# Performance work log

Hardware: AMD Instinct MI355X
Metric: run time of the kernel (lower is better)

The kernel has to match this reference:

```python
import jax, jax.numpy as jnp
import numpy as np

B, DIM, T = 8, 512, 4096
INTER = 1536
K = 7
DIL = 1
EPS = 1e-6
LS_INIT = 1e-6


def _ste(x, q):
    # straight-through estimator: forward uses q, gradient flows through x
    return x + jax.lax.stop_gradient(q - x)


def _weight_quant(w):
    # BitNet b1.58 ternary weight quant with per-tensor scale = mean(|w|)
    s = jnp.clip(jnp.mean(jnp.abs(w)), 1e-5, None)
    q = jnp.clip(jnp.round(w / s), -1.0, 1.0) * s
    return _ste(w, q)


def _act_quant(x, axis):
    # per-token int8 absmax quant along `axis`
    s = 127.0 / jnp.clip(jnp.max(jnp.abs(x), axis=axis, keepdims=True), 1e-5, None)
    q = jnp.clip(jnp.round(x * s), -128.0, 127.0) / s
    return _ste(x, q)


def setup_inputs() -> dict:
    key = jax.random.key(0)
    ks = jax.random.split(key, 5)
    return {
        "x": jax.random.normal(ks[0], (B, DIM, T), dtype=jnp.float32),
        "dw_w": jax.random.normal(ks[1], (DIM, 1, K), dtype=jnp.float32) * 0.1,
        "dw_b": jnp.zeros((DIM,), jnp.float32),
        "ln_g": jnp.ones((DIM,), jnp.float32),
        "ln_b": jnp.zeros((DIM,), jnp.float32),
        "w1": jax.random.normal(ks[2], (INTER, DIM), dtype=jnp.float32) * (1.0 / np.sqrt(DIM)),
        "b1": jnp.zeros((INTER,), jnp.float32),
        "w2": jax.random.normal(ks[3], (DIM, INTER), dtype=jnp.float32) * (1.0 / np.sqrt(INTER)),
        "b2": jnp.zeros((DIM,), jnp.float32),
        "gamma": LS_INIT * jnp.ones((DIM,), jnp.float32),
    }


def reference(x, dw_w, dw_b, ln_g, ln_b, w1, b1, w2, b2, gamma):
    residual = x  # [B, DIM, T]
    pad = (K + (DIL - 1) * (K - 1)) // 2
    # quantized depthwise conv1d
    xq = _act_quant(x, axis=1)
    wq = _weight_quant(dw_w)  # [DIM, 1, K]
    y = jax.lax.conv_general_dilated(
        xq, wq, window_strides=(1,), padding=[(pad, pad)],
        rhs_dilation=(DIL,), dimension_numbers=("NCH", "OIH", "NCH"),
        feature_group_count=DIM,
    ) + dw_b[None, :, None]
    y = y.transpose(0, 2, 1)  # [B, T, DIM]
    # LayerNorm over channels
    mu = jnp.mean(y, axis=-1, keepdims=True)
    var = jnp.var(y, axis=-1, keepdims=True)
    y = (y - mu) * jax.lax.rsqrt(var + EPS) * ln_g + ln_b
    # BitLinear 1 -> GELU -> BitLinear 2
    h = jnp.einsum("btc,fc->btf", _act_quant(y, -1), _weight_quant(w1)) + b1
    h = jax.nn.gelu(h, approximate=False)
    o = jnp.einsum("btf,cf->btc", _act_quant(h, -1), _weight_quant(w2)) + b2
    o = gamma * o
    return residual + o.transpose(0, 2, 1)  # [B, DIM, T]
```

## Files before the change

kernel.cpp:

```cpp
#include <hip/hip_runtime.h>
#include <hip/hip_bf16.h>

#define BATCH 8
#define DIM   512
#define TLEN  4096
#define INTER 1536
#define NTOK  (BATCH*TLEN)

#define QH 15.875f
#define DH (1.0f/15.875f)

typedef __attribute__((ext_vector_type(4))) float f32x4;
typedef __attribute__((ext_vector_type(8))) short s16x8;
typedef __attribute__((ext_vector_type(4))) int   i32x4;
typedef signed char i8;

__device__ __forceinline__ float bf2f(short s) {
  unsigned u = ((unsigned)(unsigned short)s) << 16;
  return __uint_as_float(u);
}
__device__ __forceinline__ short f2bf(float f) {
  union { __hip_bfloat16 h; unsigned short u; } cv;
  cv.h = __float2bfloat16(f);
  return (short)cv.u;
}
__device__ __forceinline__ void async16(void* lds, const void* g) {
  __builtin_amdgcn_global_load_lds((const __attribute__((address_space(1))) void*)g,
                                   (__attribute__((address_space(3))) void*)lds, 16, 0, 0);
}
__device__ __forceinline__ float gelu_sig(float h) {
  float e = __builtin_amdgcn_exp2f(-2.4554669f * h);
  return h * __builtin_amdgcn_rcpf(1.f + e);
}

__global__ __launch_bounds__(256)
void reduce_abs3_k(const float* __restrict__ w1, const float* __restrict__ w2,
                   const float* __restrict__ dww, float* __restrict__ ws) {
  const int b = blockIdx.x, tid = threadIdx.x;
  const float* w; int n, nb, lb; float* part;
  if (b < 128)      { w = w1;  n = INTER * DIM; nb = 128; lb = b;       part = ws + 16; }
  else if (b < 256) { w = w2;  n = INTER * DIM; nb = 128; lb = b - 128; part = ws + 144; }
  else              { w = dww; n = DIM * 7;     nb = 8;   lb = b - 256; part = ws + 272; }
  float s = 0.f;
  for (int i = lb * 256 + tid; i < n; i += nb * 256) s += fabsf(w[i]);
  #pragma unroll
  for (int off = 32; off; off >>= 1) s += __shfl_xor(s, off);
  __shared__ float ls[4];
  if ((tid & 63) == 0) ls[tid >> 6] = s;
  __syncthreads();
  if (tid == 0) part[lb] = ls[0] + ls[1] + ls[2] + ls[3];
}

__global__ void finalize_scales_k(float* __restrict__ ws) {
  const int tid = threadIdx.x;
  const int seg = tid >> 6, lane = tid & 63;
  float s;
  if (seg == 0)      s = ws[16 + lane] + ws[16 + 64 + lane];
  else if (seg == 1) s = ws[144 + lane] + ws[144 + 64 + lane];
  else               s = (lane < 8) ? ws[272 + lane] : 0.f;
  #pragma unroll
  for (int off = 32; off; off >>= 1) s += __shfl_xor(s, off);
  if (lane == 0) {
    if (seg == 0)      ws[0] = fmaxf(s / 786432.f, 1e-5f);
    else if (seg == 1) ws[1] = fmaxf(s / 786432.f, 1e-5f);
    else               ws[2] = fmaxf(s / 3584.f, 1e-5f);
  }
}

__global__ __launch_bounds__(256)
void quant_w8_both_k(const float* __restrict__ w1, const float* __restrict__ w2,
                     const float* __restrict__ sc,
                     i8* __restrict__ w1q, i8* __restrict__ w2q) {
  const int bid = blockIdx.x;
  if (bid < 3072) {
    int i = bid * 256 + threadIdx.x;
    w1q[i] = (i8)(int)fminf(fmaxf(rintf(w1[i] / sc[0]), -1.f), 1.f);
  } else {
    int i = (bid - 3072) * 256 + threadIdx.x;
    w2q[i] = (i8)(int)fminf(fmaxf(rintf(w2[i] / sc[1]), -1.f), 1.f);
  }
}

__global__ __launch_bounds__(256)
void amax_k(const float* __restrict__ x, float* __restrict__ amax) {
  const int tid = threadIdx.x;
  const int b = blockIdx.y;
  const int t0 = blockIdx.x * 128;
  const int tg = tid & 31, grp = tid >> 5;
  const float* xb = x + ((size_t)b * DIM + grp * 64) * TLEN + t0 + tg * 4;
  f32x4 m = {0.f, 0.f, 0.f, 0.f};
  for (int c = 0; c < 64; ++c) {
    f32x4 v = *(const f32x4*)(xb + (size_t)c * TLEN);
    #pragma unroll
    for (int e = 0; e < 4; ++e) m[e] = fmaxf(m[e], fabsf(v[e]));
  }
  __shared__ f32x4 pm[8][32];
  pm[grp][tg] = m;
  __syncthreads();
  if (tid < 32) {
    f32x4 r = pm[0][tid];
    #pragma unroll
    for (int g = 1; g < 8; ++g)
      #pragma unroll
      for (int e = 0; e < 4; ++e) r[e] = fmaxf(r[e], pm[g][tid][e]);
    *(f32x4*)&amax[(size_t)b * TLEN + t0 + tid * 4] = r;
  }
}

__global__ __launch_bounds__(256)
void conv_ln_quant_k(const float* __restrict__ x, const float* __restrict__ dww,
                     const float* __restrict__ dwb, const float* __restrict__ lng,
                     const float* __restrict__ lnb, const float* __restrict__ amax,
                     const float* __restrict__ scales, i8* __restrict__ yq,
                     float* __restrict__ siy) {
  __shared__ i8   xq[512 * 52];
  __shared__ short ly[32 * 512];
  __shared__ float sx[40], sxi[40];
  const int tid = threadIdx.x;
  const int b = blockIdx.y;
  const int t0 = blockIdx.x * 32;

  if (tid < 40) {
    int tg = t0 - 4 + tid;
    float a = (tg >= 0 && tg < TLEN) ? amax[(size_t)b * TLEN + tg] : 1.f;
    float m = fmaxf(a, 1e-5f);
    sx[tid] = 127.f / m;
    sxi[tid] = m * (1.f / 127.f);
  }
  __syncthreads();

  const bool interior = (t0 >= 4) && (t0 + 36 <= TLEN);
  #pragma unroll 4
  for (int p = 0; p < 20; ++p) {
    const int g = p * 256 + tid;
    const int c = g / 10;
    const int ch = g - c * 10;
    const float* xr = x + ((size_t)b * DIM + c) * TLEN + (t0 - 4) + ch * 4;
    f32x4 L;
    if (interior) {
      L = *(const f32x4*)xr;
    } else {
      #pragma unroll
      for (int e = 0; e < 4; ++e) {
        int tg = t0 - 4 + ch * 4 + e;
        L[e] = (tg >= 0 && tg < TLEN) ? xr[e] : 0.f;
      }
    }
    const f32x4 S = *(const f32x4*)&sx[ch * 4];
    unsigned pk = 0;
    #pragma unroll
    for (int e = 0; e < 4; ++e) {
      int q = (int)rintf(__builtin_amdgcn_fmed3f(L[e] * S[e], -128.f, 127.f));
      pk |= ((unsigned)(q & 255)) << (8 * e);
    }
    *(unsigned*)(xq + c * 52 + ch * 4) = pk;
  }
  __syncthreads();

  {
    const float sdw = scales[2];
    const float rs = 1.f / sdw;
    const int c0 = tid * 2;
    float w0[7], w1v[7];
    #pragma unroll
    for (int k = 0; k < 7; ++k) {
      w0[k]  = fminf(fmaxf(rintf(dww[c0 * 7 + k] * rs), -1.f), 1.f) * sdw;
      w1v[k] = fminf(fmaxf(rintf(dww[c0 * 7 + 7 + k] * rs), -1.f), 1.f) * sdw;
    }
    const float bias0 = dwb[c0], bias1 = dwb[c0 + 1];
    const i8* xr0 = xq + c0 * 52;
    const i8* xr1 = xr0 + 52;

    #define UNPK(src, u, Q) do {                                            \
      const unsigned v_ = *(const unsigned*)((src) + 4 * (u));              \
      const f32x4 SX_ = *(const f32x4*)&sxi[4 * (u)];                       \
      _Pragma("unroll")                                                     \
      for (int e_ = 0; e_ < 4; ++e_)                                        \
        Q[e_] = (float)((int)(v_ << (24 - 8 * e_)) >> 24) * SX_[e_];        \
    } while (0)

    f32x4 A0, A1, A2, B0, B1, B2;
    UNPK(xr0, 0, A0); UNPK(xr0, 1, A1);
    UNPK(xr1, 0, B0); UNPK(xr1, 1, B1);
    #pragma unroll 2
    for (int u = 0; u < 8; ++u) {
      UNPK(xr0, u + 2, A2);
      UNPK(xr1, u + 2, B2);
      #pragma unroll
      for (int s = 0; s < 4; ++s) {
        float a0 = bias0, a1 = bias1;
        #pragma unroll
        for (int k = 0; k < 7; ++k) {
          const int i = s + 1 + k;
          const float qa = (i < 4) ? A0[i & 3] : (i < 8) ? A1[i & 3] : A2[i & 3];
          const float qb = (i < 4) ? B0[i & 3] : (i < 8) ? B1[i & 3] : B2[i & 3];
          a0 += w0[k] * qa;
          a1 += w1v[k] * qb;
        }
        const int t = 4 * u + s;
        unsigned pk = (unsigned)(unsigned short)f2bf(a0) |
                      ((unsigned)(unsigned short)f2bf(a1) << 16);
        *(unsigned*)((char*)ly + t * 1024 + tid * 4) = pk;
      }
      A0 = A1; A1 = A2; B0 = B1; B1 = B2;
    }
    #undef UNPK
  }
  __syncthreads();

  const int lane = tid & 63, w = tid >> 6;
  float gg[8], bb[8];
  #pragma unroll
  for (int j = 0; j < 8; ++j) { gg[j] = lng[lane * 8 + j]; bb[j] = lnb[lane * 8 + j]; }
  for (int i = 0; i < 8; ++i) {
    const int t = w * 8 + i;
    s16x8 v = *(const s16x8*)((char*)ly + t * 1024 + lane * 16);
    float f[8];
    float s = 0.f, sq = 0.f;
    #pragma unroll
    for (int j = 0; j < 8; ++j) { f[j] = bf2f(v[j]); s += f[j]; sq += f[j] * f[j]; }
    #pragma unroll
    for (int off = 32; off; off >>= 1) { s += __shfl_xor(s, off); sq += __shfl_xor(sq, off); }
    const float mu = s * (1.f / 512.f);
    const float var = sq * (1.f / 512.f) - mu * mu;
    const float rstd = rsqrtf(var + 1e-6f);
    float amx = 0.f;
    #pragma unroll
    for (int j = 0; j < 8; ++j) {
      f[j] = (f[j] - mu) * rstd * gg[j] + bb[j];
      amx = fmaxf(amx, fabsf(f[j]));
    }
    #pragma unroll
    for (int off = 32; off; off >>= 1) amx = fmaxf(amx, __shfl_xor(amx, off));
    const float m = fmaxf(amx, 1e-5f);
    const float ss = 127.f / m;
    const int tok = b * TLEN + t0 + t;
    if (lane == 0) siy[tok] = m * (1.f / 127.f);
    unsigned lo = 0, hi = 0;
    #pragma unroll
    for (int j = 0; j < 4; ++j) {
      int q = (int)fminf(fmaxf(rintf(f[j] * ss), -128.f), 127.f);
      lo |= ((unsigned)(q & 255)) << (8 * j);
    }
    #pragma unroll
    for (int j = 4; j < 8; ++j) {
      int q = (int)fminf(fmaxf(rintf(f[j] * ss), -128.f), 127.f);
      hi |= ((unsigned)(q & 255)) << (8 * (j - 4));
    }
    uint2 pk; pk.x = lo; pk.y = hi;
    const int tl = t & 7;
    const int ch = (lane >> 1) ^ tl;
    *(uint2*)(yq + (size_t)tok * DIM + ch * 16 + (lane & 1) * 8) = pk;
  }
}

__global__ __launch_bounds__(512)
void fused_ffn_k(const i8* __restrict__ yq, const i8* __restrict__ w1q,
                 const i8* __restrict__ w2q, const float* __restrict__ b1,
                 const float* __restrict__ b2, const float* __restrict__ gamma,
                 const float* __restrict__ siy, const float* __restrict__ scales,
                 const float* __restrict__ x, float* __restrict__ out) {
  __shared__ i8 smem[163840];
  i8* const yql = smem;
  i8* const hql = smem + 65536;
  const int tid = threadIdx.x;
  const int t0 = blockIdx.x * 64;
  const int lane = tid & 63, w = tid >> 6;
  const int lc = lane & 15, lg = lane >> 4;
  const int srow_q = lane >> 2, schunk = lane & 3;
  i8* const w1s = smem + 32768 + w * 4096;
  i8* const w2s = smem + w * 8192;

  #pragma unroll
  for (int l = 0; l < 4; ++l)
    async16(yql + l * 8192 + tid * 16, yq + (size_t)t0 * DIM + l * 8192 + tid * 16);

  #define STAGE1(buf, s) do {                                                 \
    const int ftp_ = (s) >> 3, kt_ = (s) & 7;                                 \
    _Pragma("unroll")                                                         \
    for (int q_ = 0; q_ < 2; ++q_) {                                          \
      const int rr_ = q_ * 16 + srow_q;                                       \
      const int sc_ = schunk ^ ((rr_ >> 1) & 3);                              \
      async16(w1s + (buf) * 2048 + q_ * 1024 + lane * 16,                     \
              w1q + (size_t)(ftp_ * 256 + w * 32 + rr_) * DIM + kt_ * 64 + sc_ * 16); \
    }                                                                         \
  } while (0)

  STAGE1(0, 0);
  STAGE1(1, 1);
  asm volatile("" ::: "memory");
  asm volatile("s_waitcnt vmcnt(2)" ::: "memory");
  __builtin_amdgcn_s_barrier();

  #define LDAF1(F, buf)                                                       \
    _Pragma("unroll")                                                         \
    for (int i_ = 0; i_ < 2; ++i_) {                                          \
      const int ar_ = i_ * 16 + lc;                                           \
      F[i_] = *(const i32x4*)(w1s + (buf) * 2048 + ar_ * 64 +                 \
                              ((lg ^ ((ar_ >> 1) & 3)) << 4));                \
    }

  i32x4 by[8][4];
  #pragma unroll
  for (int kt = 0; kt < 8; ++kt)
    #pragma unroll
    for (int j = 0; j < 4; ++j) {
      const int tok = j * 16 + lc;
      by[kt][j] = *(const i32x4*)(yql + tok * 512 +
                                  (((kt * 4 + lg) ^ (tok & 7)) << 4));
    }

  i32x4 afP[2], afQ[2];
  LDAF1(afP, 0)
  const float sw1 = scales[0];
  float sy[4];
  #pragma unroll
  for (int j = 0; j < 4; ++j) sy[j] = siy[t0 + j * 16 + lc] * sw1;

  i32x4 acc[2][4] = {};
  for (int ftp = 0; ftp < 3; ++ftp) {
    #pragma unroll
    for (int kt = 0; kt < 8; ++kt) {
      const int s = ftp * 8 + kt;
      if (ftp < 2 || kt < 6) {
        STAGE1(kt & 1, s + 2);
        asm volatile("s_waitcnt vmcnt(2)" ::: "memory");
      } else {
        asm volatile("s_waitcnt vmcnt(0)" ::: "memory");
      }
      if (ftp < 2 || kt < 7) {
        if (kt & 1) { LDAF1(afP, 0) } else { LDAF1(afQ, 1) }
      }
      __builtin_amdgcn_sched_barrier(0);
      __builtin_amdgcn_s_setprio(1);
      #pragma unroll
      for (int i_ = 0; i_ < 2; ++i_)
        #pragma unroll
        for (int j_ = 0; j_ < 4; ++j_)
          acc[i_][j_] = __builtin_amdgcn_mfma_i32_16x16x64_i8(
              (kt & 1) ? afQ[i_] : afP[i_], by[kt][j_], acc[i_][j_], 0, 0, 0);
      __builtin_amdgcn_s_setprio(0);
      if (kt == 7) {
        #pragma unroll
        for (int i_ = 0; i_ < 2; ++i_) {
          const int f0_ = ftp * 256 + w * 32 + i_ * 16 + lg * 4;
          const int cb_ = ftp * 16 + w * 2 + i_;
          float b1v_[4];
          #pragma unroll
          for (int r_ = 0; r_ < 4; ++r_) b1v_[r_] = b1[f0_ + r_];
          #pragma unroll
          for (int j_ = 0; j_ < 4; ++j_) {
            const int tok_ = j_ * 16 + lc;
            unsigned pk_ = 0;
            #pragma unroll
            for (int r_ = 0; r_ < 4; ++r_) {
              float hv_ = fmaf((float)acc[i_][j_][r_], sy[j_], b1v_[r_]);
              float gv_ = gelu_sig(hv_);
              int q_ = (int)rintf(__builtin_amdgcn_fmed3f(gv_ * QH, -128.f, 127.f));
              pk_ |= ((unsigned)(q_ & 255)) << (8 * r_);
              acc[i_][j_][r_] = 0;
            }
            *(unsigned*)(hql + tok_ * 1536 + (((cb_ ^ (tok_ & 7)) << 4) + lg * 4)) = pk_;
          }
        }
      }
    }
  }
  #undef STAGE1
  #undef LDAF1
  __syncthreads();

  #define STAGE2(buf, s) do {                                                 \
    _Pragma("unroll")                                                         \
    for (int q_ = 0; q_ < 4; ++q_) {                                          \
      const int rr_ = q_ * 16 + srow_q;                                       \
      const int sc_ = schunk ^ ((rr_ >> 1) & 3);                              \
      async16(w2s + (buf) * 4096 + q_ * 1024 + lane * 16,                     \
              w2q + (size_t)(w * 64 + rr_) * INTER + (s) * 64 + sc_ * 16);    \
    }                                                                         \
  } while (0)
  #define LDAF2(F, buf)                                                       \
    _Pragma("unroll")                                                         \
    for (int i_ = 0; i_ < 4; ++i_) {                                          \
      const int ar_ = i_ * 16 + lc;                                           \
      F[i_] = *(const i32x4*)(w2s + (buf) * 4096 + ar_ * 64 +                 \
                              ((lg ^ ((ar_ >> 1) & 3)) << 4));                \
    }
  #define LDBF_H(B, s)                                                        \
    _Pragma("unroll")                                                         \
    for (int j_ = 0; j_ < 4; ++j_) {                                          \
      const int tok_ = j_ * 16 + lc;                                          \
      B[j_] = *(const i32x4*)(hql + tok_ * 1536 +                             \
                              ((((s) * 4 + lg) ^ (tok_ & 7)) << 4));          \
    }

  STAGE2(0, 0);
  STAGE2(1, 1);
  asm volatile("" ::: "memory");
  asm volatile("s_waitcnt vmcnt(4)" ::: "memory");
  i32x4 a3fP[4], a3fQ[4], b3fP[4], b3fQ[4];
  LDAF2(a3fP, 0)
  LDBF_H(b3fP, 0)
  i32x4 a3[4][4] = {};

  #define P3_STEP(s, FC, FN, BC, BN) do {                                     \
    if ((s) + 2 < 24) {                                                       \
      STAGE2((s) & 1, (s) + 2);                                               \
      asm volatile("s_waitcnt vmcnt(4)" ::: "memory");                        \
    } else {                                                                  \
      asm volatile("s_waitcnt vmcnt(0)" ::: "memory");                        \
    }                                                                         \
    if ((s) + 1 < 24) {                                                       \
      LDAF2(FN, ((s) + 1) & 1)                                                \
      LDBF_H(BN, (s) + 1)                                                     \
    }                                                                         \
    __builtin_amdgcn_sched_barrier(0);                                        \
    __builtin_amdgcn_s_setprio(1);                                            \
    _Pragma("unroll")                                                         \
    for (int i_ = 0; i_ < 4; ++i_)                                            \
      _Pragma("unroll")                                                       \
      for (int j_ = 0; j_ < 4; ++j_)                                          \
        a3[i_][j_] = __builtin_amdgcn_mfma_i32_16x16x64_i8(FC[i_], BC[j_],    \
                                                           a3[i_][j_], 0, 0, 0); \
    __builtin_amdgcn_s_setprio(0);                                            \
  } while (0)

  for (int sp = 0; sp < 12; ++sp) {
    P3_STEP(2 * sp,     a3fP, a3fQ, b3fP, b3fQ);
    P3_STEP(2 * sp + 1, a3fQ, a3fP, b3fQ, b3fP);
  }
  #undef P3_STEP
  #undef STAGE2
  #undef LDAF2
  #undef LDBF_H

  const float dq = scales[1] * DH;
  #pragma unroll
  for (int i = 0; i < 4; ++i) {
    const int c0 = w * 64 + i * 16 + lg * 4;
    #pragma unroll
    for (int j = 0; j < 4; ++j) {
      const int tok = t0 + j * 16 + lc;
      const int bb = tok >> 12;
      const int tt = tok & 4095;
      #pragma unroll
      for (int r = 0; r < 4; ++r) {
        const int c = c0 + r;
        float o = (float)a3[i][j][r] * dq + b2[c];
        size_t idx = ((size_t)(bb * DIM + c)) * TLEN + tt;
        out[idx] = x[idx] + gamma[c] * o;
      }
    }
  }
}

extern "C" void kernel_launch(void* const* d_in, const int* in_sizes, int n_in,
                              void* d_out, int out_size, void* d_ws, size_t ws_size,
                              hipStream_t stream) {
  const float* x    = (const float*)d_in[0];
  const float* dww  = (const float*)d_in[1];
  const float* dwb  = (const float*)d_in[2];
  const float* lng  = (const float*)d_in[3];
  const float* lnb  = (const float*)d_in[4];
  const float* w1   = (const float*)d_in[5];
  const float* b1   = (const float*)d_in[6];
  const float* w2   = (const float*)d_in[7];
  const float* b2   = (const float*)d_in[8];
  const float* gam  = (const float*)d_in[9];
  float* out = (float*)d_out;

  const size_t NEEDED = 18616320;
  if (ws_size < NEEDED) return;

  char* ws = (char*)d_ws;
  float* scales = (float*)ws;
  float* amax   = (float*)(ws + 4096);
  float* siy    = (float*)(ws + 135168);
  i8* w1q       = (i8*)(ws + 266240);
  i8* w2q       = (i8*)(ws + 1052672);
  i8* yq        = (i8*)(ws + 1839104);

  reduce_abs3_k<<<264, 256, 0, stream>>>(w1, w2, dww, scales);
  finalize_scales_k<<<1, 192, 0, stream>>>(scales);
  quant_w8_both_k<<<6144, 256, 0, stream>>>(w1, w2, scales, w1q, w2q);
  amax_k<<<dim3(TLEN / 128, BATCH), 256, 0, stream>>>(x, amax);
  conv_ln_quant_k<<<dim3(TLEN / 32, BATCH), 256, 0, stream>>>(x, dww, dwb, lng, lnb,
                                                              amax, scales, yq, siy);
  fused_ffn_k<<<NTOK / 64, 512, 0, stream>>>(yq, w1q, w2q, b1, b2, gam, siy,
                                             scales, x, out);
}
```

Measured before the change: 148.0 us.

## Deepen W1 staging pipeline to four buffers in fused FFN stage 1

Raises the number of in-flight async W1 tile loads in the first GEMM of the fused FFN from two to four stages. The two extra buffers reuse the yq LDS region once its B fragments have been read into registers, which needs an extra barrier. Waitcnt thresholds are adjusted to match the deeper queue, and the ftp loop is fully unrolled so buffer indices are compile-time. The aim is to hide more global-load latency behind the MFMAs, at the cost of an added sync point and higher code size and register pressure.

```diff
diff --git a/kernel.cpp b/kernel.cpp
--- a/kernel.cpp
+++ b/kernel.cpp
@@ -32,6 +32,8 @@
   float e = __builtin_amdgcn_exp2f(-2.4554669f * h);
   return h * __builtin_amdgcn_rcpf(1.f + e);
 }
+
+#define VMW(N) asm volatile("s_waitcnt vmcnt(" #N ")" ::: "memory")
 
 __global__ __launch_bounds__(256)
 void reduce_abs3_k(const float* __restrict__ w1, const float* __restrict__ w2,
@@ -268,8 +270,10 @@
   const int lane = tid & 63, w = tid >> 6;
   const int lc = lane & 15, lg = lane >> 4;
   const int srow_q = lane >> 2, schunk = lane & 3;
-  i8* const w1s = smem + 32768 + w * 4096;
   i8* const w2s = smem + w * 8192;
+
+  #define W1SADDR(buf) ((buf) < 2 ? (smem + 32768 + w * 4096 + (buf) * 2048)  \
+                                  : (smem + w * 4096 + ((buf) - 2) * 2048))
 
   #pragma unroll
   for (int l = 0; l < 4; ++l)
@@ -277,11 +281,12 @@
 
   #define STAGE1(buf, s) do {                                                 \
     const int ftp_ = (s) >> 3, kt_ = (s) & 7;                                 \
+    i8* wb_ = (i8*)W1SADDR(buf);                                              \
     _Pragma("unroll")                                                         \
     for (int q_ = 0; q_ < 2; ++q_) {                                          \
       const int rr_ = q_ * 16 + srow_q;                                       \
       const int sc_ = schunk ^ ((rr_ >> 1) & 3);                              \
-      async16(w1s + (buf) * 2048 + q_ * 1024 + lane * 16,                     \
+      async16(wb_ + q_ * 1024 + lane * 16,                                    \
               w1q + (size_t)(ftp_ * 256 + w * 32 + rr_) * DIM + kt_ * 64 + sc_ * 16); \
     }                                                                         \
   } while (0)
@@ -289,28 +294,34 @@
   STAGE1(0, 0);
   STAGE1(1, 1);
   asm volatile("" ::: "memory");
-  asm volatile("s_waitcnt vmcnt(2)" ::: "memory");
+  VMW(4);
   __builtin_amdgcn_s_barrier();
+
+  i32x4 by[8][4];
+  #pragma unroll
+  for (int kt = 0; kt < 8; ++kt)
+    #pragma unroll
+    for (int j = 0; j < 4; ++j) {
+      const int tok = j * 16 + lc;
+      by[kt][j] = *(const i32x4*)(yql + tok * 512 +
+                                  (((kt * 4 + lg) ^ (tok & 7)) << 4));
+    }
+  asm volatile("s_waitcnt lgkmcnt(0)" ::: "memory");
+  __builtin_amdgcn_s_barrier();
+
+  STAGE1(2, 2);
+  STAGE1(3, 3);
 
   #define LDAF1(F, buf)                                                       \
     _Pragma("unroll")                                                         \
     for (int i_ = 0; i_ < 2; ++i_) {                                          \
       const int ar_ = i_ * 16 + lc;                                           \
-      F[i_] = *(const i32x4*)(w1s + (buf) * 2048 + ar_ * 64 +                 \
+      F[i_] = *(const i32x4*)(W1SADDR(buf) + ar_ * 64 +                       \
                               ((lg ^ ((ar_ >> 1) & 3)) << 4));                \
     }
 
-  i32x4 by[8][4];
-  #pragma unroll
-  for (int kt = 0; kt < 8; ++kt)
-    #pragma unroll
-    for (int j = 0; j < 4; ++j) {
-      const int tok = j * 16 + lc;
-      by[kt][j] = *(const i32x4*)(yql + tok * 512 +
-                                  (((kt * 4 + lg) ^ (tok & 7)) << 4));
-    }
-
   i32x4 afP[2], afQ[2];
+  VMW(6);
   LDAF1(afP, 0)
   const float sw1 = scales[0];
   float sy[4];
@@ -318,18 +329,20 @@
   for (int j = 0; j < 4; ++j) sy[j] = siy[t0 + j * 16 + lc] * sw1;
 
   i32x4 acc[2][4] = {};
+  #pragma unroll
   for (int ftp = 0; ftp < 3; ++ftp) {
     #pragma unroll
     for (int kt = 0; kt < 8; ++kt) {
       const int s = ftp * 8 + kt;
-      if (ftp < 2 || kt < 6) {
-        STAGE1(kt & 1, s + 2);
-        asm volatile("s_waitcnt vmcnt(2)" ::: "memory");
-      } else {
-        asm volatile("s_waitcnt vmcnt(0)" ::: "memory");
-      }
-      if (ftp < 2 || kt < 7) {
-        if (kt & 1) { LDAF1(afP, 0) } else { LDAF1(afQ, 1) }
+      if (s + 4 < 24) {
+        STAGE1(s & 3, s + 4);
+        VMW(6);
+      } else if (s == 20) { VMW(4); }
+      else if (s == 21)   { VMW(2); }
+      else if (s == 22)   { VMW(0); }
+      if (s + 1 < 24) {
+        if (kt & 1) { LDAF1(afP, ((s + 1) & 3)) }
+        else        { LDAF1(afQ, ((s + 1) & 3)) }
       }
       __builtin_amdgcn_sched_barrier(0);
       __builtin_amdgcn_s_setprio(1);
@@ -368,6 +381,7 @@
   }
   #undef STAGE1
   #undef LDAF1
+  #undef W1SADDR
   __syncthreads();
 
   #define STAGE2(buf, s) do {                                                 \
@@ -397,7 +411,7 @@
   STAGE2(0, 0);
   STAGE2(1, 1);
   asm volatile("" ::: "memory");
-  asm volatile("s_waitcnt vmcnt(4)" ::: "memory");
+  VMW(4);
   i32x4 a3fP[4], a3fQ[4], b3fP[4], b3fQ[4];
   LDAF2(a3fP, 0)
   LDBF_H(b3fP, 0)
@@ -406,9 +420,9 @@
   #define P3_STEP(s, FC, FN, BC, BN) do {                                     \
     if ((s) + 2 < 24) {                                                       \
       STAGE2((s) & 1, (s) + 2);                                               \
-      asm volatile("s_waitcnt vmcnt(4)" ::: "memory");                        \
+      VMW(4);                                                                 \
     } else {                                                                  \
-      asm volatile("s_waitcnt vmcnt(0)" ::: "memory");                        \
+      VMW(0);                                                                 \
     }                                                                         \
     if ((s) + 1 < 24) {                                                       \
       LDAF2(FN, ((s) + 1) & 1)                                                \
```

New measurement: 148.4 us. About the same (+0.3%).

## Split fused FFN across 16 waves with single-buffered per-wave weight staging

Applied to the files above, without the earlier changes.

Doubles the fused FFN block to 1024 threads (16 waves), so each wave covers half as many output rows in both GEMMs. The per-wave weight staging drops to one 2 KB buffer: the next slice is issued right after the current fragments are read from LDS and waited on at the top of the next step. Activation fragments are now reread from LDS every step instead of being held in registers. The aim is to cut per-wave register pressure and add latency hiding through more waves, but the single buffer leaves only a few MFMAs between issuing a global load and waiting on it. The `__launch_bounds__(1024, 4)` hint may also force an aggressive register cap and cause spills.

```diff
diff --git a/kernel.cpp b/kernel.cpp
--- a/kernel.cpp
+++ b/kernel.cpp
@@ -32,6 +32,9 @@
   float e = __builtin_amdgcn_exp2f(-2.4554669f * h);
   return h * __builtin_amdgcn_rcpf(1.f + e);
 }
+
+#define VMW(N) asm volatile("s_waitcnt vmcnt(" #N ")" ::: "memory")
+#define LKW0() asm volatile("s_waitcnt lgkmcnt(0)" ::: "memory")
 
 __global__ __launch_bounds__(256)
 void reduce_abs3_k(const float* __restrict__ w1, const float* __restrict__ w2,
@@ -254,7 +257,7 @@
   }
 }
 
-__global__ __launch_bounds__(512)
+__global__ __launch_bounds__(1024, 4)
 void fused_ffn_k(const i8* __restrict__ yq, const i8* __restrict__ w1q,
                  const i8* __restrict__ w2q, const float* __restrict__ b1,
                  const float* __restrict__ b2, const float* __restrict__ gamma,
@@ -267,51 +270,28 @@
   const int t0 = blockIdx.x * 64;
   const int lane = tid & 63, w = tid >> 6;
   const int lc = lane & 15, lg = lane >> 4;
-  const int srow_q = lane >> 2, schunk = lane & 3;
-  i8* const w1s = smem + 32768 + w * 4096;
-  i8* const w2s = smem + w * 8192;
-
-  #pragma unroll
-  for (int l = 0; l < 4; ++l)
-    async16(yql + l * 8192 + tid * 16, yq + (size_t)t0 * DIM + l * 8192 + tid * 16);
-
-  #define STAGE1(buf, s) do {                                                 \
+  const int srow = lane >> 2, schk = lane & 3;
+  i8* const myst = smem + 32768 + w * 2048;
+
+  async16(yql + tid * 16, yq + (size_t)t0 * DIM + tid * 16);
+  async16(yql + 16384 + tid * 16, yq + (size_t)t0 * DIM + 16384 + tid * 16);
+
+  #define STAGE1(s) do {                                                      \
     const int ftp_ = (s) >> 3, kt_ = (s) & 7;                                 \
     _Pragma("unroll")                                                         \
     for (int q_ = 0; q_ < 2; ++q_) {                                          \
-      const int rr_ = q_ * 16 + srow_q;                                       \
-      const int sc_ = schunk ^ ((rr_ >> 1) & 3);                              \
-      async16(w1s + (buf) * 2048 + q_ * 1024 + lane * 16,                     \
-              w1q + (size_t)(ftp_ * 256 + w * 32 + rr_) * DIM + kt_ * 64 + sc_ * 16); \
+      const int rr_ = q_ * 16 + srow;                                         \
+      const int sc_ = schk ^ ((rr_ >> 1) & 3);                                \
+      async16(myst + q_ * 1024 + lane * 16,                                   \
+              w1q + (size_t)(ftp_ * 512 + w * 32 + rr_) * DIM + kt_ * 64 + sc_ * 16); \
     }                                                                         \
   } while (0)
 
-  STAGE1(0, 0);
-  STAGE1(1, 1);
+  STAGE1(0);
   asm volatile("" ::: "memory");
-  asm volatile("s_waitcnt vmcnt(2)" ::: "memory");
+  VMW(2);
   __builtin_amdgcn_s_barrier();
 
-  #define LDAF1(F, buf)                                                       \
-    _Pragma("unroll")                                                         \
-    for (int i_ = 0; i_ < 2; ++i_) {                                          \
-      const int ar_ = i_ * 16 + lc;                                           \
-      F[i_] = *(const i32x4*)(w1s + (buf) * 2048 + ar_ * 64 +                 \
-                              ((lg ^ ((ar_ >> 1) & 3)) << 4));                \
-    }
-
-  i32x4 by[8][4];
-  #pragma unroll
-  for (int kt = 0; kt < 8; ++kt)
-    #pragma unroll
-    for (int j = 0; j < 4; ++j) {
-      const int tok = j * 16 + lc;
-      by[kt][j] = *(const i32x4*)(yql + tok * 512 +
-                                  (((kt * 4 + lg) ^ (tok & 7)) << 4));
-    }
-
-  i32x4 afP[2], afQ[2];
-  LDAF1(afP, 0)
   const float sw1 = scales[0];
   float sy[4];
   #pragma unroll
@@ -322,29 +302,34 @@
     #pragma unroll
     for (int kt = 0; kt < 8; ++kt) {
       const int s = ftp * 8 + kt;
-      if (ftp < 2 || kt < 6) {
-        STAGE1(kt & 1, s + 2);
-        asm volatile("s_waitcnt vmcnt(2)" ::: "memory");
-      } else {
-        asm volatile("s_waitcnt vmcnt(0)" ::: "memory");
-      }
-      if (ftp < 2 || kt < 7) {
-        if (kt & 1) { LDAF1(afP, 0) } else { LDAF1(afQ, 1) }
-      }
+      VMW(0);
+      i32x4 af[2], bf[4];
+      #pragma unroll
+      for (int i_ = 0; i_ < 2; ++i_) {
+        const int ar = i_ * 16 + lc;
+        af[i_] = *(const i32x4*)(myst + ar * 64 + ((lg ^ ((ar >> 1) & 3)) << 4));
+      }
+      #pragma unroll
+      for (int j_ = 0; j_ < 4; ++j_) {
+        const int tok = j_ * 16 + lc;
+        bf[j_] = *(const i32x4*)(yql + tok * 512 + (((kt * 4 + lg) ^ (tok & 7)) << 4));
+      }
+      LKW0();
       __builtin_amdgcn_sched_barrier(0);
+      if (s + 1 < 24) STAGE1(s + 1);
       __builtin_amdgcn_s_setprio(1);
       #pragma unroll
       for (int i_ = 0; i_ < 2; ++i_)
         #pragma unroll
         for (int j_ = 0; j_ < 4; ++j_)
-          acc[i_][j_] = __builtin_amdgcn_mfma_i32_16x16x64_i8(
-              (kt & 1) ? afQ[i_] : afP[i_], by[kt][j_], acc[i_][j_], 0, 0, 0);
+          acc[i_][j_] = __builtin_amdgcn_mfma_i32_16x16x64_i8(af[i_], bf[j_],
+                                                              acc[i_][j_], 0, 0, 0);
       __builtin_amdgcn_s_setprio(0);
       if (kt == 7) {
         #pragma unroll
         for (int i_ = 0; i_ < 2; ++i_) {
-          const int f0_ = ftp * 256 + w * 32 + i_ * 16 + lg * 4;
-          const int cb_ = ftp * 16 + w * 2 + i_;
+          const int f0_ = ftp * 512 + w * 32 + i_ * 16 + lg * 4;
+          const int cb_ = ftp * 32 + w * 2 + i_;
           float b1v_[4];
           #pragma unroll
           for (int r_ = 0; r_ < 4; ++r_) b1v_[r_] = b1[f0_ + r_];
@@ -367,77 +352,52 @@
     }
   }
   #undef STAGE1
-  #undef LDAF1
-  __syncthreads();
-
-  #define STAGE2(buf, s) do {                                                 \
+  __syncthreads();
+
+  #define STAGE2(s) do {                                                      \
     _Pragma("unroll")                                                         \
-    for (int q_ = 0; q_ < 4; ++q_) {                                          \
-      const int rr_ = q_ * 16 + srow_q;                                       \
-      const int sc_ = schunk ^ ((rr_ >> 1) & 3);                              \
-      async16(w2s + (buf) * 4096 + q_ * 1024 + lane * 16,                     \
-              w2q + (size_t)(w * 64 + rr_) * INTER + (s) * 64 + sc_ * 16);    \
+    for (int q_ = 0; q_ < 2; ++q_) {                                          \
+      const int rr_ = q_ * 16 + srow;                                         \
+      const int sc_ = schk ^ ((rr_ >> 1) & 3);                                \
+      async16(myst + q_ * 1024 + lane * 16,                                   \
+              w2q + (size_t)(w * 32 + rr_) * INTER + (s) * 64 + sc_ * 16);    \
     }                                                                         \
   } while (0)
-  #define LDAF2(F, buf)                                                       \
-    _Pragma("unroll")                                                         \
-    for (int i_ = 0; i_ < 4; ++i_) {                                          \
-      const int ar_ = i_ * 16 + lc;                                           \
-      F[i_] = *(const i32x4*)(w2s + (buf) * 4096 + ar_ * 64 +                 \
-                              ((lg ^ ((ar_ >> 1) & 3)) << 4));                \
-    }
-  #define LDBF_H(B, s)                                                        \
-    _Pragma("unroll")                                                         \
-    for (int j_ = 0; j_ < 4; ++j_) {                                          \
-      const int tok_ = j_ * 16 + lc;                                          \
-      B[j_] = *(const i32x4*)(hql + tok_ * 1536 +                             \
-                              ((((s) * 4 + lg) ^ (tok_ & 7)) << 4));          \
-    }
-
-  STAGE2(0, 0);
-  STAGE2(1, 1);
-  asm volatile("" ::: "memory");
-  asm volatile("s_waitcnt vmcnt(4)" ::: "memory");
-  i32x4 a3fP[4], a3fQ[4], b3fP[4], b3fQ[4];
-  LDAF2(a3fP, 0)
-  LDBF_H(b3fP, 0)
-  i32x4 a3[4][4] = {};
-
-  #define P3_STEP(s, FC, FN, BC, BN) do {                                     \
-    if ((s) + 2 < 24) {                                                       \
-      STAGE2((s) & 1, (s) + 2);                                               \
-      asm volatile("s_waitcnt vmcnt(4)" ::: "memory");                        \
-    } else {                                                                  \
-      asm volatile("s_waitcnt vmcnt(0)" ::: "memory");                        \
-    }                                                                         \
-    if ((s) + 1 < 24) {                                                       \
-      LDAF2(FN, ((s) + 1) & 1)                                                \
-      LDBF_H(BN, (s) + 1)                                                     \
-    }                                                                         \
-    __builtin_amdgcn_sched_barrier(0);                                        \
-    __builtin_amdgcn_s_setprio(1);                                            \
-    _Pragma("unroll")                                                         \
-    for (int i_ = 0; i_ < 4; ++i_)                                            \
-      _Pragma("unroll")                                                       \
-      for (int j_ = 0; j_ < 4; ++j_)                                          \
-        a3[i_][j_] = __builtin_amdgcn_mfma_i32_16x16x64_i8(FC[i_], BC[j_],    \
-                                                           a3[i_][j_], 0, 0, 0); \
-    __builtin_amdgcn_s_setprio(0);                                            \
-  } while (0)
-
-  for (int sp = 0; sp < 12; ++sp) {
-    P3_STEP(2 * sp,     a3fP, a3fQ, b3fP, b3fQ);
-    P3_STEP(2 * sp + 1, a3fQ, a3fP, b3fQ, b3fP);
-  }
-  #undef P3_STEP
+
+  STAGE2(0);
+  i32x4 a3[2][4] = {};
+  #pragma unroll 4
+  for (int s = 0; s < 24; ++s) {
+    VMW(0);
+    i32x4 af[2], bf[4];
+    #pragma unroll
+    for (int i_ = 0; i_ < 2; ++i_) {
+      const int ar = i_ * 16 + lc;
+      af[i_] = *(const i32x4*)(myst + ar * 64 + ((lg ^ ((ar >> 1) & 3)) << 4));
+    }
+    #pragma unroll
+    for (int j_ = 0; j_ < 4; ++j_) {
+      const int tok = j_ * 16 + lc;
+      bf[j_] = *(const i32x4*)(hql + tok * 1536 + (((s * 4 + lg) ^ (tok & 7)) << 4));
+    }
+    LKW0();
+    __builtin_amdgcn_sched_barrier(0);
+    if (s + 1 < 24) STAGE2(s + 1);
+    __builtin_amdgcn_s_setprio(1);
+    #pragma unroll
+    for (int i_ = 0; i_ < 2; ++i_)
+      #pragma unroll
+      for (int j_ = 0; j_ < 4; ++j_)
+        a3[i_][j_] = __builtin_amdgcn_mfma_i32_16x16x64_i8(af[i_], bf[j_],
+                                                           a3[i_][j_], 0, 0, 0);
+    __builtin_amdgcn_s_setprio(0);
+  }
   #undef STAGE2
-  #undef LDAF2
-  #undef LDBF_H
 
   const float dq = scales[1] * DH;
   #pragma unroll
-  for (int i = 0; i < 4; ++i) {
-    const int c0 = w * 64 + i * 16 + lg * 4;
+  for (int i = 0; i < 2; ++i) {
+    const int c0 = w * 32 + i * 16 + lg * 4;
     #pragma unroll
     for (int j = 0; j < 4; ++j) {
       const int tok = t0 + j * 16 + lc;
@@ -486,6 +446,6 @@
   amax_k<<<dim3(TLEN / 128, BATCH), 256, 0, stream>>>(x, amax);
   conv_ln_quant_k<<<dim3(TLEN / 32, BATCH), 256, 0, stream>>>(x, dww, dwb, lng, lnb,
                                                               amax, scales, yq, siy);
-  fused_ffn_k<<<NTOK / 64, 512, 0, stream>>>(yq, w1q, w2q, b1, b2, gam, siy,
-                                             scales, x, out);
-}
+  fused_ffn_k<<<NTOK / 64, 1024, 0, stream>>>(yq, w1q, w2q, b1, b2, gam, siy,
+                                              scales, x, out);
+}
```

Result: slower. 169.9 us (+14.8%).
